# Performance work log

Hardware: AMD Instinct MI355X
Metric: run time of the kernel (lower is better)

Reference implementation:

```python
import jax, jax.numpy as jnp
import numpy as np

TEMPERATURE = 1.0 / 0.07  # fixed (temperature_trainable=False)
B, D = 256, 65536


def setup_inputs() -> dict:
    key = jax.random.key(0)
    kA, kB = jax.random.split(key)
    feat_A = jax.random.normal(kA, (B, D), dtype=jnp.float32)
    feat_B = jax.random.normal(kB, (B, D), dtype=jnp.float32)
    # L2-normalize (standard for contrastive features; keeps exp(logits) finite)
    feat_A = feat_A / jnp.linalg.norm(feat_A, axis=-1, keepdims=True)
    feat_B = feat_B / jnp.linalg.norm(feat_B, axis=-1, keepdims=True)
    return {"feat_A": feat_A, "feat_B": feat_B}


def reference(feat_A, feat_B):
    # logits[i, j] = <A_i, B_j> * temperature   -- [B, B]
    logits = jnp.einsum("id,jd->ij", feat_A, feat_B) * TEMPERATURE
    pos_logits = jnp.diagonal(logits)  # [B]
    # margin=0.0, dcl=False, index=None -> neg_mask is all True, so
    # log(sum_j exp(logits)) is a full-row/col logsumexp (stable form of exp->sum->log)
    neg_A2B = jax.nn.logsumexp(logits, axis=1)  # A -> B classification
    neg_B2A = jax.nn.logsumexp(logits, axis=0)  # B -> A classification
    loss_A2B = jnp.mean(neg_A2B - pos_logits)
    loss_B2A = jnp.mean(neg_B2A - pos_logits)
    return (loss_A2B + loss_B2A) * 0.5
```

## Files before the change

### kernel.cpp

```cpp
#include <hip/hip_runtime.h>


#define D_DIM 65536
#define B_DIM 256
#define C_CHUNKS 32
#define KC (D_DIM / C_CHUNKS)
#define KCW (KC / 4)

constexpr float TEMP = 1.0f / 0.07f;

typedef short short8 __attribute__((ext_vector_type(8)));
typedef float floatx4 __attribute__((ext_vector_type(4)));

__device__ inline unsigned fbits(float f) { return __builtin_bit_cast(unsigned, f); }

__device__ inline unsigned pkbf(float lo, float hi) {
  unsigned ul = fbits(lo) + 0x8000u;
  unsigned uh = fbits(hi) + 0x8000u;
  return __builtin_amdgcn_perm(uh, ul, 0x07060302);
}

__device__ inline short8 cvt_frag(float4 a, float4 b) {
  union { unsigned u[4]; short8 s; } r;
  r.u[0] = pkbf(a.x, a.y);
  r.u[1] = pkbf(a.z, a.w);
  r.u[2] = pkbf(b.x, b.y);
  r.u[3] = pkbf(b.z, b.w);
  return r.s;
}

__global__ __launch_bounds__(256, 2) void gemm_stream(
    const float* __restrict__ A, const float* __restrict__ Bm,
    float* __restrict__ partials, float* __restrict__ out) {
  if (blockIdx.x == 0 && threadIdx.x == 0) *out = 0.f;

  const int bid = blockIdx.x;
  const int chunk = bid >> 4;
  const int tile = bid & 15;
  const int mt = (tile & 3) * 64;
  const int nt = (tile >> 2) * 64;

  const int t = threadIdx.x;
  const int lane = t & 63;
  const int w = t >> 6;
  const int r16 = lane & 15;
  const int q = lane >> 4;

  const size_t kb = (size_t)chunk * KC + (size_t)w * KCW;

  const float* pa[4];
  const float* pb[4];
#pragma unroll
  for (int f = 0; f < 4; ++f) {
    pa[f] = A  + (size_t)(mt + f * 16 + r16) * D_DIM + kb + q * 8;
    pb[f] = Bm + (size_t)(nt + f * 16 + r16) * D_DIM + kb + q * 8;
  }

  floatx4 acc[16];
#pragma unroll
  for (int i = 0; i < 16; ++i) acc[i] = (floatx4)0.f;

  float4 xa[8], xb[8], ya[8], yb[8];

#define LOADSET(da, db, off)                                   \
  {                                                            \
    _Pragma("unroll") for (int f = 0; f < 4; ++f) {            \
      da[2 * f]     = *(const float4*)(pa[f] + (off));         \
      da[2 * f + 1] = *(const float4*)(pa[f] + (off) + 4);     \
      db[2 * f]     = *(const float4*)(pb[f] + (off));         \
      db[2 * f + 1] = *(const float4*)(pb[f] + (off) + 4);     \
    }                                                          \
  }

#define COMPUTESET(da, db)                                                    \
  {                                                                           \
    short8 af[4], bf[4];                                                      \
    _Pragma("unroll") for (int f = 0; f < 4; ++f) {                           \
      af[f] = cvt_frag(da[2 * f], da[2 * f + 1]);                             \
      bf[f] = cvt_frag(db[2 * f], db[2 * f + 1]);                             \
    }                                                                         \
    _Pragma("unroll") for (int mb = 0; mb < 4; ++mb)                          \
        _Pragma("unroll") for (int nb = 0; nb < 4; ++nb)                      \
            acc[mb * 4 + nb] = __builtin_amdgcn_mfma_f32_16x16x32_bf16(       \
                af[mb], bf[nb], acc[mb * 4 + nb], 0, 0, 0);                   \
  }

  LOADSET(xa, xb, 0)
#pragma unroll 1
  for (int g = 0; g < KCW / 64; ++g) {
    LOADSET(ya, yb, g * 64 + 32)
    COMPUTESET(xa, xb)
    if (g + 1 < KCW / 64) LOADSET(xa, xb, g * 64 + 64)
    COMPUTESET(ya, yb)
  }

  __shared__ float red[4][4096];
#pragma unroll
  for (int mb = 0; mb < 4; ++mb)
#pragma unroll
    for (int nb = 0; nb < 4; ++nb)
#pragma unroll
      for (int r = 0; r < 4; ++r)
        red[w][(mb * 16 + q * 4 + r) * 64 + nb * 16 + r16] = acc[mb * 4 + nb][r];
  __syncthreads();

  float* outp = partials + (size_t)chunk * (B_DIM * B_DIM);
#pragma unroll
  for (int jj = 0; jj < 16; ++jj) {
    const int e = jj * 256 + t;
    const float v = red[0][e] + red[1][e] + red[2][e] + red[3][e];
    const int row = e >> 6, col = e & 63;
    outp[(size_t)(mt + row) * B_DIM + nt + col] = v;
  }
#undef LOADSET
#undef COMPUTESET
}

__global__ __launch_bounds__(256, 4) void reduce_all(
    const float* __restrict__ partials, float* __restrict__ out) {
  const int i = blockIdx.x;
  const int j = threadIdx.x;

  float s = 0.f;
  const float* p = partials + (size_t)i * B_DIM + j;
#pragma unroll
  for (int c = 0; c < C_CHUNKS; ++c) s += p[(size_t)c * (B_DIM * B_DIM)];
  const float lgr = s * TEMP;

  __shared__ float posv;
  if (j == i) posv = lgr;

  float s2 = 0.f;
  const float* p2 = partials + (size_t)j * B_DIM + i;
#pragma unroll
  for (int c = 0; c < C_CHUNKS; ++c) s2 += p2[(size_t)c * (B_DIM * B_DIM)];
  const float lgc = s2 * TEMP;

  float e1 = expf(lgr);
  float e2 = expf(lgc);
#pragma unroll
  for (int off = 32; off > 0; off >>= 1) {
    e1 += __shfl_down(e1, off);
    e2 += __shfl_down(e2, off);
  }
  __shared__ float w1[4], w2[4];
  if ((j & 63) == 0) { w1[j >> 6] = e1; w2[j >> 6] = e2; }
  __syncthreads();
  if (j == 0) {
    const float rs = w1[0] + w1[1] + w1[2] + w1[3];
    const float cs = w2[0] + w2[1] + w2[2] + w2[3];
    atomicAdd(out, (logf(rs) + logf(cs) - 2.f * posv) * (0.5f / 256.f));
  }
}

extern "C" void kernel_launch(void* const* d_in, const int* in_sizes, int n_in,
                              void* d_out, int out_size, void* d_ws, size_t ws_size,
                              hipStream_t stream) {
  (void)in_sizes; (void)n_in; (void)out_size; (void)ws_size;
  const float* A = (const float*)d_in[0];
  const float* Bm = (const float*)d_in[1];
  float* out = (float*)d_out;
  float* partials = (float*)d_ws;

  gemm_stream<<<16 * C_CHUNKS, 256, 0, stream>>>(A, Bm, partials, out);
  reduce_all<<<B_DIM, B_DIM, 0, stream>>>(partials, out);
}
```

Before: 188.5 us.

## Split 64x64 tiles across waves in M/N, double K-chunks, single-pass reduction

Each wave now owns a 32x32 sub-tile of the block's 64x64 output and covers the whole K chunk, instead of all four waves splitting K and summing through shared memory. This drops the LDS reduction and cuts accumulator registers, which allows higher occupancy (launch bounds 4). K chunks double to 64 so there are more blocks. The reduction kernel now reads partials once, accumulates column exp-sums with atomics and finishes the column logsumexp in the last block. In exchange each block re-reads A and B rows with less reuse per wave and writes twice as many partials.

Measured after the change: 255.1 us. 1.35x slower.

```diff
diff --git a/kernel.cpp b/kernel.cpp
--- a/kernel.cpp
+++ b/kernel.cpp
@@ -3,9 +3,8 @@
 
 #define D_DIM 65536
 #define B_DIM 256
-#define C_CHUNKS 32
+#define C_CHUNKS 64
 #define KC (D_DIM / C_CHUNKS)
-#define KCW (KC / 4)
 
 constexpr float TEMP = 1.0f / 0.07f;
 
@@ -15,109 +14,104 @@
 __device__ inline unsigned fbits(float f) { return __builtin_bit_cast(unsigned, f); }
 
 __device__ inline unsigned pkbf(float lo, float hi) {
-  unsigned ul = fbits(lo) + 0x8000u;
-  unsigned uh = fbits(hi) + 0x8000u;
-  return __builtin_amdgcn_perm(uh, ul, 0x07060302);
+  return __builtin_amdgcn_perm(fbits(hi) + 0x8000u, fbits(lo) + 0x8000u, 0x07060302);
 }
 
-__device__ inline short8 cvt_frag(float4 a, float4 b) {
+__device__ inline short8 cvt_frag(float4 lo, float4 hi) {
   union { unsigned u[4]; short8 s; } r;
-  r.u[0] = pkbf(a.x, a.y);
-  r.u[1] = pkbf(a.z, a.w);
-  r.u[2] = pkbf(b.x, b.y);
-  r.u[3] = pkbf(b.z, b.w);
+  r.u[0] = pkbf(lo.x, lo.y);
+  r.u[1] = pkbf(lo.z, lo.w);
+  r.u[2] = pkbf(hi.x, hi.y);
+  r.u[3] = pkbf(hi.z, hi.w);
   return r.s;
 }
 
-__global__ __launch_bounds__(256, 2) void gemm_stream(
+__global__ __launch_bounds__(256, 4) void gemm_stream(
     const float* __restrict__ A, const float* __restrict__ Bm,
-    float* __restrict__ partials, float* __restrict__ out) {
-  if (blockIdx.x == 0 && threadIdx.x == 0) *out = 0.f;
+    float* __restrict__ partials, float* __restrict__ colsum,
+    float* __restrict__ out, unsigned* __restrict__ counter) {
+  const int bid = blockIdx.x;
+  const int t = threadIdx.x;
+  if (bid == 0) {
+    colsum[t] = 0.f;
+    if (t == 0) { *out = 0.f; *counter = 0u; }
+  }
 
-  const int bid = blockIdx.x;
-  const int chunk = bid >> 4;
-  const int tile = bid & 15;
+  const int chunk = bid & (C_CHUNKS - 1);
+  const int tile = bid >> 6;
   const int mt = (tile & 3) * 64;
   const int nt = (tile >> 2) * 64;
 
-  const int t = threadIdx.x;
   const int lane = t & 63;
   const int w = t >> 6;
+  const int wm = mt + (w & 1) * 32;
+  const int wn = nt + (w >> 1) * 32;
   const int r16 = lane & 15;
   const int q = lane >> 4;
 
-  const size_t kb = (size_t)chunk * KC + (size_t)w * KCW;
+  const size_t kb = (size_t)chunk * KC + (size_t)q * 8;
+  const float* pa0 = A + (size_t)(wm + r16) * D_DIM + kb;
+  const float* pa1 = pa0 + (size_t)16 * D_DIM;
+  const float* pb0 = Bm + (size_t)(wn + r16) * D_DIM + kb;
+  const float* pb1 = pb0 + (size_t)16 * D_DIM;
 
-  const float* pa[4];
-  const float* pb[4];
-#pragma unroll
-  for (int f = 0; f < 4; ++f) {
-    pa[f] = A  + (size_t)(mt + f * 16 + r16) * D_DIM + kb + q * 8;
-    pb[f] = Bm + (size_t)(nt + f * 16 + r16) * D_DIM + kb + q * 8;
+  floatx4 acc00 = (floatx4)0.f, acc01 = (floatx4)0.f;
+  floatx4 acc10 = (floatx4)0.f, acc11 = (floatx4)0.f;
+
+  float4 x[8], y[8];
+
+#define LOADSET(d, off)                                  \
+  {                                                      \
+    d[0] = *(const float4*)(pa0 + (off));                \
+    d[1] = *(const float4*)(pa0 + (off) + 4);            \
+    d[2] = *(const float4*)(pa1 + (off));                \
+    d[3] = *(const float4*)(pa1 + (off) + 4);            \
+    d[4] = *(const float4*)(pb0 + (off));                \
+    d[5] = *(const float4*)(pb0 + (off) + 4);            \
+    d[6] = *(const float4*)(pb1 + (off));                \
+    d[7] = *(const float4*)(pb1 + (off) + 4);            \
   }
 
-  floatx4 acc[16];
-#pragma unroll
-  for (int i = 0; i < 16; ++i) acc[i] = (floatx4)0.f;
-
-  float4 xa[8], xb[8], ya[8], yb[8];
-
-#define LOADSET(da, db, off)                                   \
-  {                                                            \
-    _Pragma("unroll") for (int f = 0; f < 4; ++f) {            \
-      da[2 * f]     = *(const float4*)(pa[f] + (off));         \
-      da[2 * f + 1] = *(const float4*)(pa[f] + (off) + 4);     \
-      db[2 * f]     = *(const float4*)(pb[f] + (off));         \
-      db[2 * f + 1] = *(const float4*)(pb[f] + (off) + 4);     \
-    }                                                          \
+#define COMPUTESET(d)                                                       \
+  {                                                                         \
+    short8 a0 = cvt_frag(d[0], d[1]);                                       \
+    short8 a1 = cvt_frag(d[2], d[3]);                                       \
+    short8 b0 = cvt_frag(d[4], d[5]);                                       \
+    short8 b1 = cvt_frag(d[6], d[7]);                                       \
+    acc00 = __builtin_amdgcn_mfma_f32_16x16x32_bf16(a0, b0, acc00, 0, 0, 0);\
+    acc01 = __builtin_amdgcn_mfma_f32_16x16x32_bf16(a0, b1, acc01, 0, 0, 0);\
+    acc10 = __builtin_amdgcn_mfma_f32_16x16x32_bf16(a1, b0, acc10, 0, 0, 0);\
+    acc11 = __builtin_amdgcn_mfma_f32_16x16x32_bf16(a1, b1, acc11, 0, 0, 0);\
   }
 
-#define COMPUTESET(da, db)                                                    \
-  {                                                                           \
-    short8 af[4], bf[4];                                                      \
-    _Pragma("unroll") for (int f = 0; f < 4; ++f) {                           \
-      af[f] = cvt_frag(da[2 * f], da[2 * f + 1]);                             \
-      bf[f] = cvt_frag(db[2 * f], db[2 * f + 1]);                             \
-    }                                                                         \
-    _Pragma("unroll") for (int mb = 0; mb < 4; ++mb)                          \
-        _Pragma("unroll") for (int nb = 0; nb < 4; ++nb)                      \
-            acc[mb * 4 + nb] = __builtin_amdgcn_mfma_f32_16x16x32_bf16(       \
-                af[mb], bf[nb], acc[mb * 4 + nb], 0, 0, 0);                   \
-  }
-
-  LOADSET(xa, xb, 0)
+  LOADSET(x, 0)
 #pragma unroll 1
-  for (int g = 0; g < KCW / 64; ++g) {
-    LOADSET(ya, yb, g * 64 + 32)
-    COMPUTESET(xa, xb)
-    if (g + 1 < KCW / 64) LOADSET(xa, xb, g * 64 + 64)
-    COMPUTESET(ya, yb)
-  }
-
-  __shared__ float red[4][4096];
-#pragma unroll
-  for (int mb = 0; mb < 4; ++mb)
-#pragma unroll
-    for (int nb = 0; nb < 4; ++nb)
-#pragma unroll
-      for (int r = 0; r < 4; ++r)
-        red[w][(mb * 16 + q * 4 + r) * 64 + nb * 16 + r16] = acc[mb * 4 + nb][r];
-  __syncthreads();
-
-  float* outp = partials + (size_t)chunk * (B_DIM * B_DIM);
-#pragma unroll
-  for (int jj = 0; jj < 16; ++jj) {
-    const int e = jj * 256 + t;
-    const float v = red[0][e] + red[1][e] + red[2][e] + red[3][e];
-    const int row = e >> 6, col = e & 63;
-    outp[(size_t)(mt + row) * B_DIM + nt + col] = v;
+  for (int g = 0; g < KC / 64; ++g) {
+    LOADSET(y, g * 64 + 32)
+    COMPUTESET(x)
+    if (g + 1 < KC / 64) LOADSET(x, g * 64 + 64)
+    COMPUTESET(y)
   }
 #undef LOADSET
 #undef COMPUTESET
+
+  float* op = partials + (size_t)chunk * (B_DIM * B_DIM);
+  const floatx4* accs[4] = {&acc00, &acc01, &acc10, &acc11};
+#pragma unroll
+  for (int fa = 0; fa < 2; ++fa)
+#pragma unroll
+    for (int fb = 0; fb < 2; ++fb) {
+      const floatx4 a = *accs[fa * 2 + fb];
+      const int col = wn + fb * 16 + r16;
+#pragma unroll
+      for (int r = 0; r < 4; ++r)
+        op[(size_t)(wm + fa * 16 + q * 4 + r) * B_DIM + col] = a[r];
+    }
 }
 
-__global__ __launch_bounds__(256, 4) void reduce_all(
-    const float* __restrict__ partials, float* __restrict__ out) {
+__global__ __launch_bounds__(256, 2) void reduce_all(
+    const float* __restrict__ partials, float* __restrict__ colsum,
+    float* __restrict__ out, unsigned* __restrict__ counter) {
   const int i = blockIdx.x;
   const int j = threadIdx.x;
 
@@ -125,31 +119,39 @@
   const float* p = partials + (size_t)i * B_DIM + j;
 #pragma unroll
   for (int c = 0; c < C_CHUNKS; ++c) s += p[(size_t)c * (B_DIM * B_DIM)];
-  const float lgr = s * TEMP;
+  const float lg = s * TEMP;
 
   __shared__ float posv;
-  if (j == i) posv = lgr;
+  if (j == i) posv = lg;
 
-  float s2 = 0.f;
-  const float* p2 = partials + (size_t)j * B_DIM + i;
+  const float e = expf(lg);
+  atomicAdd(&colsum[j], e);
+
+  float r = e;
 #pragma unroll
-  for (int c = 0; c < C_CHUNKS; ++c) s2 += p2[(size_t)c * (B_DIM * B_DIM)];
-  const float lgc = s2 * TEMP;
+  for (int off = 32; off > 0; off >>= 1) r += __shfl_down(r, off);
+  __shared__ float wsum[4];
+  if ((j & 63) == 0) wsum[j >> 6] = r;
+  __threadfence();
+  __syncthreads();
 
-  float e1 = expf(lgr);
-  float e2 = expf(lgc);
+  __shared__ bool last;
+  if (j == 0) {
+    const float rowsum = wsum[0] + wsum[1] + wsum[2] + wsum[3];
+    atomicAdd(out, (logf(rowsum) - 2.f * posv) * (0.5f / 256.f));
+    last = (atomicAdd(counter, 1u) == B_DIM - 1);
+  }
+  __syncthreads();
+
+  if (last) {
+    __threadfence();
+    float cl = logf(colsum[j]);
 #pragma unroll
-  for (int off = 32; off > 0; off >>= 1) {
-    e1 += __shfl_down(e1, off);
-    e2 += __shfl_down(e2, off);
-  }
-  __shared__ float w1[4], w2[4];
-  if ((j & 63) == 0) { w1[j >> 6] = e1; w2[j >> 6] = e2; }
-  __syncthreads();
-  if (j == 0) {
-    const float rs = w1[0] + w1[1] + w1[2] + w1[3];
-    const float cs = w2[0] + w2[1] + w2[2] + w2[3];
-    atomicAdd(out, (logf(rs) + logf(cs) - 2.f * posv) * (0.5f / 256.f));
+    for (int off = 32; off > 0; off >>= 1) cl += __shfl_down(cl, off);
+    if ((j & 63) == 0) wsum[j >> 6] = cl;
+    __syncthreads();
+    if (j == 0)
+      atomicAdd(out, (wsum[0] + wsum[1] + wsum[2] + wsum[3]) * (0.5f / 256.f));
   }
 }
 
@@ -160,8 +162,11 @@
   const float* A = (const float*)d_in[0];
   const float* Bm = (const float*)d_in[1];
   float* out = (float*)d_out;
+
   float* partials = (float*)d_ws;
+  float* colsum = partials + (size_t)C_CHUNKS * B_DIM * B_DIM;
+  unsigned* counter = (unsigned*)(colsum + B_DIM);
 
-  gemm_stream<<<16 * C_CHUNKS, 256, 0, stream>>>(A, Bm, partials, out);
-  reduce_all<<<B_DIM, B_DIM, 0, stream>>>(partials, out);
+  gemm_stream<<<16 * C_CHUNKS, 256, 0, stream>>>(A, Bm, partials, colsum, out, counter);
+  reduce_all<<<B_DIM, B_DIM, 0, stream>>>(partials, colsum, out, counter);
 }
```
